# Optimization experiments

Measured on AMD Instinct MI355X. Metric: run time of the kernel, lower is better.

## Reference

```python
import jax, jax.numpy as jnp
import numpy as np

HEAD_DIM = 128  # kv_channels


def setup_inputs() -> dict:
    key = jax.random.key(0)
    k1, k2, k3 = jax.random.split(key, 3)
    s, b, h, d = 2048, 2, 16, HEAD_DIM
    return {
        "query_layer": jax.random.normal(k1, (s, b, h, d), dtype=jnp.float32),
        "key_layer": jax.random.normal(k2, (s, b, h, d), dtype=jnp.float32),
        "value_layer": jax.random.normal(k3, (s, b, h, d), dtype=jnp.float32),
    }


def reference(query_layer, key_layer, value_layer):
    # shapes: [seq, batch, heads, head_dim]
    s, b, h, d = query_layer.shape
    norm = 1.0 / jnp.sqrt(jnp.asarray(d, dtype=jnp.float32))
    # QK^T with 1/sqrt(d) scaling -> [b, h, q, k]
    scores = jnp.einsum("qbhd,kbhd->bhqk", query_layer, key_layer) * norm
    # softmax computed in float32 (TorchScaledMaskedSoftmax casts to float)
    probs = jax.nn.softmax(scores.astype(jnp.float32), axis=-1).astype(query_layer.dtype)
    # dropout p=0.0 -> identity
    # AV: [b,h,q,k] x [k,b,h,d] -> [q,b,h,d]
    ctx = jnp.einsum("bhqk,kbhd->qbhd", probs, value_layer)
    # [seq, batch, heads*head_dim]
    return ctx.reshape(s, b, h * d)
```

## Files before the change

### kernel.cpp

```cpp
#include <hip/hip_runtime.h>
#include <stdint.h>

#define S_LEN 2048
#define BHN   32
#define HD    128

typedef __attribute__((ext_vector_type(8))) short short8;
typedef __attribute__((ext_vector_type(16))) float f32x16;

__device__ __forceinline__ unsigned short f2bf(float f) {
    union { float f; uint32_t u; } v; v.f = f;
    return (unsigned short)((v.u + 0x7FFFu + ((v.u >> 16) & 1u)) >> 16);
}
__device__ __forceinline__ uint32_t pack2bf_rhu(float a, float b) {
    union { float f; uint32_t u; } x, y; x.f = a; y.f = b;
    return ((x.u + 0x8000u) >> 16) | ((y.u + 0x8000u) & 0xFFFF0000u);
}
__device__ __forceinline__ void gll16(const void* g, const void* l) {
    __builtin_amdgcn_global_load_lds(
        (const __attribute__((address_space(1))) uint32_t*)g,
        (__attribute__((address_space(3))) uint32_t*)l, 16, 0, 0);
}

__global__ __launch_bounds__(256) void prepass_kernel(const float* __restrict__ K,
                                                      const float* __restrict__ V,
                                                      unsigned short* __restrict__ img) {
    __shared__ unsigned short vt[8192];
    const int bh = blockIdx.x & 31;
    const int kt = blockIdx.x >> 5;
    const int s0 = kt << 6;
    const int tid = threadIdx.x;
    unsigned short* base = img + ((size_t)(bh * 32 + kt) << 14);

    for (int i = tid; i < 1024; i += 256) {
        int r = i >> 4, cc = i & 15;
        const float* src = K + (size_t)(s0 + r) * 4096 + bh * 128 + cc * 8;
        float4 a = *(const float4*)src;
        float4 b = *(const float4*)(src + 4);
        short8 t;
        t[0] = (short)f2bf(a.x); t[1] = (short)f2bf(a.y);
        t[2] = (short)f2bf(a.z); t[3] = (short)f2bf(a.w);
        t[4] = (short)f2bf(b.x); t[5] = (short)f2bf(b.y);
        t[6] = (short)f2bf(b.z); t[7] = (short)f2bf(b.w);
        *(short8*)(base + r * 128 + ((cc ^ (r & 15)) << 3)) = t;
    }
    for (int i = tid; i < 1024; i += 256) {
        int r = i >> 4, cc = i & 15;
        const float* src = V + (size_t)(s0 + r) * 4096 + bh * 128 + cc * 8;
        float4 a = *(const float4*)src;
        float4 b = *(const float4*)(src + 4);
        short8 t;
        t[0] = (short)f2bf(a.x); t[1] = (short)f2bf(a.y);
        t[2] = (short)f2bf(a.z); t[3] = (short)f2bf(a.w);
        t[4] = (short)f2bf(b.x); t[5] = (short)f2bf(b.y);
        t[6] = (short)f2bf(b.z); t[7] = (short)f2bf(b.w);
        *(short8*)(vt + r * 128 + ((cc ^ (r & 15)) << 3)) = t;
    }
    __syncthreads();
    for (int i = tid; i < 1024; i += 256) {
        int rp = i >> 3, p = i & 7, cc = p ^ (rp & 7);
        int dc = rp >> 3, dl = rp & 7;
        short8 t;
#pragma unroll
        for (int j = 0; j < 8; ++j) {
            int k = cc * 8 + j;
            t[j] = (short)vt[k * 128 + ((dc ^ (k & 15)) << 3) + dl];
        }
        *(short8*)(base + 8192 + rp * 64 + (p << 3)) = t;
    }
}

__global__ __launch_bounds__(256, 2) void attn_kernel(const float* __restrict__ Q,
                                                      const unsigned short* __restrict__ img,
                                                      float* __restrict__ Out) {
    __shared__ char smem[65536];

    const int wg   = blockIdx.x;
    const int bh   = ((wg & 7) << 2) + ((wg >> 3) & 3);
    const int q0   = (wg >> 5) << 7;
    const int tid  = threadIdx.x;
    const int wave = tid >> 6, lane = tid & 63;
    const int l32  = lane & 31, h = lane >> 5;

    short8 qb[8];
    {
        const float* qp = Q + (size_t)(q0 + wave * 32 + l32) * 4096 + bh * 128 + h * 8;
#pragma unroll
        for (int ks = 0; ks < 8; ++ks) {
            float4 x = *(const float4*)(qp + ks * 16);
            float4 y = *(const float4*)(qp + ks * 16 + 4);
            short8 t;
            t[0] = (short)f2bf(x.x); t[1] = (short)f2bf(x.y);
            t[2] = (short)f2bf(x.z); t[3] = (short)f2bf(x.w);
            t[4] = (short)f2bf(y.x); t[5] = (short)f2bf(y.y);
            t[6] = (short)f2bf(y.z); t[7] = (short)f2bf(y.w);
            qb[ks] = t;
        }
    }
    asm volatile("s_waitcnt vmcnt(0)" ::: "memory");

    const char* ibase = (const char*)img + ((size_t)bh << 20);

#pragma unroll
    for (int i = 0; i < 8; ++i) {
        int c = (wave * 8 + i) << 10;
        gll16(ibase + c + (lane << 4), smem + c);
    }

    f32x16 o[4];
#pragma unroll
    for (int t = 0; t < 4; ++t) o[t] = (f32x16)(0.0f);
    float lsum = 0.0f;

    const float K1 = 0.127531021f;
    const float K2 = -11.54156036f;

    for (int it = 0; it < 32; ++it) {
        const int cur = it & 1;
        const char* bufK = smem + (cur << 15);
        const char* bufV = bufK + 16384;
        char* nb = smem + ((1 - cur) << 15);
        const char* ntile = ibase + ((size_t)((it + 1) & 31) << 15);

        asm volatile("s_barrier" ::: "memory");
#pragma unroll
        for (int i = 0; i < 8; ++i) {
            int c = (wave * 8 + i) << 10;
            gll16(ntile + c + (lane << 4), nb + c);
        }
        asm volatile("s_waitcnt vmcnt(8)\n\ts_barrier" ::: "memory");

        f32x16 sacc[2];
        sacc[0] = (f32x16)(0.0f); sacc[1] = (f32x16)(0.0f);
#pragma unroll
        for (int ks = 0; ks < 8; ++ks) {
#pragma unroll
            for (int mt = 0; mt < 2; ++mt) {
                short8 kf = *(const short8*)(bufK + (mt * 32 + l32) * 256 +
                                             (((ks * 2 + h) ^ (l32 & 15)) << 4));
                sacc[mt] = __builtin_amdgcn_mfma_f32_32x32x16_bf16(kf, qb[ks], sacc[mt], 0, 0, 0);
            }
        }

        uint32_t pka[2][4], pkb[2][4];
#pragma unroll
        for (int mt = 0; mt < 2; ++mt) {
#pragma unroll
            for (int g = 0; g < 4; ++g) {
                float p0 = __builtin_amdgcn_exp2f(fmaf(sacc[mt][4 * g + 0], K1, K2));
                float p1 = __builtin_amdgcn_exp2f(fmaf(sacc[mt][4 * g + 1], K1, K2));
                float p2 = __builtin_amdgcn_exp2f(fmaf(sacc[mt][4 * g + 2], K1, K2));
                float p3 = __builtin_amdgcn_exp2f(fmaf(sacc[mt][4 * g + 3], K1, K2));
                lsum += (p0 + p1) + (p2 + p3);
                pka[mt][g] = pack2bf_rhu(p0, p1);
                pkb[mt][g] = pack2bf_rhu(p2, p3);
            }
        }

        short8 pa[4];
#pragma unroll
        for (int ks = 0; ks < 4; ++ks) {
            const int mt = ks >> 1, gl = (ks & 1) * 2;
            uint32_t ax = pka[mt][gl],     ay = pkb[mt][gl];
            uint32_t bx = pka[mt][gl + 1], by = pkb[mt][gl + 1];
            uint32_t sax = __shfl_xor(ax, 32), say = __shfl_xor(ay, 32);
            uint32_t sbx = __shfl_xor(bx, 32), sby = __shfl_xor(by, 32);
            union { uint32_t u[4]; short8 s; } cvt;
            cvt.u[0] = h ? sbx : ax;
            cvt.u[1] = h ? sby : ay;
            cvt.u[2] = h ? bx  : sax;
            cvt.u[3] = h ? by  : say;
            pa[ks] = cvt.s;
        }

#pragma unroll
        for (int ks = 0; ks < 4; ++ks) {
#pragma unroll
            for (int t = 0; t < 4; ++t) {
                short8 vf = *(const short8*)(bufV + (t * 32 + l32) * 128 +
                                             (((ks * 2 + h) ^ (l32 & 7)) << 4));
                o[t] = __builtin_amdgcn_mfma_f32_32x32x16_bf16(pa[ks], vf, o[t], 0, 0, 0);
            }
        }
    }

    float l = lsum + __shfl_xor(lsum, 32);
    float inv = 1.0f / l;
    float* op = Out + (size_t)(q0 + wave * 32) * 4096 + bh * 128 + l32;
#pragma unroll
    for (int r = 0; r < 16; ++r) {
        const int qr = (r & 3) + 8 * (r >> 2) + 4 * h;
        float iv = __shfl(inv, qr);
#pragma unroll
        for (int t = 0; t < 4; ++t)
            op[(size_t)qr * 4096 + t * 32] = o[t][r] * iv;
    }
}

extern "C" void kernel_launch(void* const* d_in, const int* in_sizes, int n_in,
                              void* d_out, int out_size, void* d_ws, size_t ws_size,
                              hipStream_t stream) {
    const float* Q = (const float*)d_in[0];
    const float* K = (const float*)d_in[1];
    const float* V = (const float*)d_in[2];

    unsigned short* img = (unsigned short*)d_ws;

    prepass_kernel<<<1024, 256, 0, stream>>>(K, V, img);
    attn_kernel<<<512, 256, 0, stream>>>(Q, img, (float*)d_out);
}
```

Baseline: 207.3 us.

## Software-pipeline PV matmul one iteration behind QK to overlap softmax

Splits the K and V tile loads into separate double buffers and defers each tile's P·V MFMA to the next iteration, where it is issued right after that iteration's QK^T MFMAs. Each V tile is now loaded one iteration later than its K tile, and a final epilogue handles the last tile. The aim is to let the exp and bf16 packing of one tile overlap with matrix-core work from the previous tile, and to reduce the dependency stall between softmax and the PV product. It keeps pa live across iterations, which raises register pressure, and it relies on the new vmcnt and barrier ordering being correct.

```diff
diff --git a/kernel.cpp b/kernel.cpp
--- a/kernel.cpp
+++ b/kernel.cpp
@@ -102,8 +102,8 @@
     const char* ibase = (const char*)img + ((size_t)bh << 20);
 
 #pragma unroll
-    for (int i = 0; i < 8; ++i) {
-        int c = (wave * 8 + i) << 10;
+    for (int i = 0; i < 4; ++i) {
+        int c = (wave * 4 + i) << 10;
         gll16(ibase + c + (lane << 4), smem + c);
     }
 
@@ -111,22 +111,29 @@
 #pragma unroll
     for (int t = 0; t < 4; ++t) o[t] = (f32x16)(0.0f);
     float lsum = 0.0f;
+    short8 pa[4];
 
     const float K1 = 0.127531021f;
     const float K2 = -11.54156036f;
 
     for (int it = 0; it < 32; ++it) {
-        const int cur = it & 1;
-        const char* bufK = smem + (cur << 15);
-        const char* bufV = bufK + 16384;
-        char* nb = smem + ((1 - cur) << 15);
+        const char* kcur  = smem + ((it & 1) << 14);
+        char*       knext = smem + (((it + 1) & 1) << 14);
+        const char* vprev = smem + 32768 + (((it + 1) & 1) << 14);
+        char*       vnext = smem + 32768 + ((it & 1) << 14);
         const char* ntile = ibase + ((size_t)((it + 1) & 31) << 15);
+        const char* ctile = ibase + ((size_t)it << 15);
 
         asm volatile("s_barrier" ::: "memory");
 #pragma unroll
-        for (int i = 0; i < 8; ++i) {
-            int c = (wave * 8 + i) << 10;
-            gll16(ntile + c + (lane << 4), nb + c);
+        for (int i = 0; i < 4; ++i) {
+            int c = (wave * 4 + i) << 10;
+            gll16(ntile + c + (lane << 4), knext + c);
+        }
+#pragma unroll
+        for (int i = 0; i < 4; ++i) {
+            int c = (wave * 4 + i) << 10;
+            gll16(ctile + 16384 + c + (lane << 4), vnext + c);
         }
         asm volatile("s_waitcnt vmcnt(8)\n\ts_barrier" ::: "memory");
 
@@ -136,9 +143,21 @@
         for (int ks = 0; ks < 8; ++ks) {
 #pragma unroll
             for (int mt = 0; mt < 2; ++mt) {
-                short8 kf = *(const short8*)(bufK + (mt * 32 + l32) * 256 +
+                short8 kf = *(const short8*)(kcur + (mt * 32 + l32) * 256 +
                                              (((ks * 2 + h) ^ (l32 & 15)) << 4));
                 sacc[mt] = __builtin_amdgcn_mfma_f32_32x32x16_bf16(kf, qb[ks], sacc[mt], 0, 0, 0);
+            }
+        }
+
+        if (it) {
+#pragma unroll
+            for (int ks = 0; ks < 4; ++ks) {
+#pragma unroll
+                for (int t = 0; t < 4; ++t) {
+                    short8 vf = *(const short8*)(vprev + (t * 32 + l32) * 128 +
+                                                 (((ks * 2 + h) ^ (l32 & 7)) << 4));
+                    o[t] = __builtin_amdgcn_mfma_f32_32x32x16_bf16(pa[ks], vf, o[t], 0, 0, 0);
+                }
             }
         }
 
@@ -157,7 +176,6 @@
             }
         }
 
-        short8 pa[4];
 #pragma unroll
         for (int ks = 0; ks < 4; ++ks) {
             const int mt = ks >> 1, gl = (ks & 1) * 2;
@@ -172,12 +190,18 @@
             cvt.u[3] = h ? by  : say;
             pa[ks] = cvt.s;
         }
-
+    }
+
+    asm volatile("s_waitcnt vmcnt(0)" ::: "memory");
+    __builtin_amdgcn_s_barrier();
+
+    {
+        const char* vlast = smem + 32768 + 16384;
 #pragma unroll
         for (int ks = 0; ks < 4; ++ks) {
 #pragma unroll
             for (int t = 0; t < 4; ++t) {
-                short8 vf = *(const short8*)(bufV + (t * 32 + l32) * 128 +
+                short8 vf = *(const short8*)(vlast + (t * 32 + l32) * 128 +
                                              (((ks * 2 + h) ^ (l32 & 7)) << 4));
                 o[t] = __builtin_amdgcn_mfma_f32_32x32x16_bf16(pa[ks], vf, o[t], 0, 0, 0);
             }
```

Result: slower. 216.0 us (+4.2%).
